# Kernel optimization log

Hardware: AMD Instinct MI355X
Metric: run time of the kernel (lower is better)

## Reference

```python
import jax, jax.numpy as jnp
import numpy as np

B, N, E = 128, 4096, 262144  # batch, num_vertices, num_edges


def setup_inputs() -> dict:
    key = jax.random.key(0)
    k1, k2, k3, k4, k5 = jax.random.split(key, 5)
    x = jax.random.normal(k1, (B, N), dtype=jnp.float32)
    error = jax.random.normal(k2, (B, N), dtype=jnp.float32)
    w = jax.random.normal(k3, (N, N), dtype=jnp.float32) * 0.02  # dense weight matrix, masked by adj in orig
    src = jax.random.randint(k4, (E,), 0, N)
    tgt = jax.random.randint(k5, (E,), 0, N)
    edge_index = jnp.stack([src, tgt]).astype(jnp.int32)  # [2, E]
    return {"x": x, "error": error, "w": w, "edge_index": edge_index}


def reference(x, error, w, edge_index):
    # Activation f = tanh, dfdx = 1 - tanh^2 (set_activation convention).
    src, tgt = edge_index[0], edge_index[1]
    w_e = w[src, tgt]  # per-edge weight gather, [E]

    # --- PredictionMessagePassing (flow='target_to_source', aggr='add') ---
    # message: f(x_j) * weight with x_j = x[tgt]; aggregated at src nodes.
    fx_t = jnp.tanh(x[:, tgt])                          # [B, E]
    mu = jnp.zeros_like(x).at[:, src].add(fx_t * w_e)   # scatter-add -> [B, N]

    # --- GradientMessagePassing (flow='source_to_target', aggr='add') ---
    # message: dfdx(x_i) * error_j * weight with x_i = x[tgt], error_j = error[src];
    # aggregated at tgt nodes; update: error - aggr_out.
    dfdx_t = 1.0 - fx_t * fx_t                          # [B, E]
    aggr = jnp.zeros_like(x).at[:, tgt].add(dfdx_t * error[:, src] * w_e)
    dEdx = error - aggr                                 # [B, N]

    return mu, dEdx
```

## Files before the change

kernel.cpp:

```cpp
#include <hip/hip_runtime.h>
#include <hip/hip_fp16.h>
#include <math.h>

#define B    128
#define NV   4096
#define NE   262144
#define CAP  192
#define KSC  128
#define EPB  2048
#define NS   8192
#define SCOLS 64


__device__ inline float2 h2f(unsigned u) {
    __half2 h;
    *reinterpret_cast<unsigned*>(&h) = u;
    return __half22float2(h);
}
__device__ inline __half2 u2h2(unsigned u) {
    __half2 h;
    *reinterpret_cast<unsigned*>(&h) = u;
    return h;
}

__global__ __launch_bounds__(256)
void k_hist(const int* __restrict__ ei, const float* __restrict__ w,
            unsigned* __restrict__ hist, ushort* __restrict__ wst) {
    __shared__ unsigned shm[NS];
    const int t = threadIdx.x, blk = blockIdx.x;
#pragma unroll
    for (int i = 0; i < NS / 256; ++i) shm[t + 256 * i] = 0u;
    __syncthreads();
    const int base = blk * EPB + t;
    int sn[8], tn[8];
#pragma unroll
    for (int i = 0; i < 8; ++i) {
        const int e = base + 256 * i;
        sn[i] = ei[e];
        tn[i] = ei[NE + e];
    }
    ushort wh[8];
#pragma unroll
    for (int i = 0; i < 8; ++i)
        wh[i] = __half_as_ushort(__float2half_rn(w[(size_t)sn[i] * NV + tn[i]]));
#pragma unroll
    for (int i = 0; i < 8; ++i) {
        atomicAdd(&shm[sn[i]], 1u);
        atomicAdd(&shm[4096 + tn[i]], 1u);
    }
#pragma unroll
    for (int i = 0; i < 8; ++i)
        wst[base + 256 * i] = wh[i];
    __syncthreads();
    unsigned* hrow = hist + (size_t)blk * NS;
#pragma unroll
    for (int i = 0; i < NS / 256; ++i) hrow[t + 256 * i] = shm[t + 256 * i];
}

__global__ __launch_bounds__(256)
void k_ts(const float* __restrict__ x, const float* __restrict__ err,
          ushort* __restrict__ Th, ushort* __restrict__ Eh,
          const unsigned* __restrict__ hist, unsigned* __restrict__ off,
          unsigned* __restrict__ count) {
    __shared__ unsigned shm[NS];
    const int t = threadIdx.x, blk = blockIdx.x;

    if (blk < 512) {
        float* tile0 = (float*)shm;
        float* tile1 = tile0 + 1056;
        const int n0 = (blk & 127) * 32;
        const int b0 = (blk >> 7) * 32;
        const int a = t & 31, c0 = t >> 5;
#pragma unroll
        for (int r = 0; r < 4; ++r) {
            int c = c0 + 8 * r;
            int gi = (b0 + c) * NV + (n0 + a);
            tile0[c * 33 + a] = tanhf(x[gi]);
            tile1[c * 33 + a] = err[gi];
        }
        __syncthreads();
#pragma unroll
        for (int r = 0; r < 4; ++r) {
            int c = c0 + 8 * r;
            int go = (n0 + c) * B + (b0 + a);
            Th[go] = __half_as_ushort(__float2half_rn(tile0[a * 33 + c]));
            Eh[go] = __half_as_ushort(__float2half_rn(tile1[a * 33 + c]));
        }
    } else {
        unsigned* p = shm;
        const int n0 = (blk - 512) * SCOLS;
#pragma unroll
        for (int i = 0; i < (KSC * SCOLS) / 256; ++i) {
            int l = t + 256 * i;
            p[l] = hist[(size_t)(l >> 6) * NS + n0 + (l & 63)];
        }
        __syncthreads();
        const int col = t >> 2, seg = t & 3;
        unsigned s = 0;
#pragma unroll
        for (int j = 0; j < KSC / 4; ++j) s += p[(seg * (KSC / 4) + j) * SCOLS + col];
        unsigned inc = s;
        unsigned v1 = __shfl_up(inc, 1, 4); if (seg >= 1) inc += v1;
        unsigned v2 = __shfl_up(inc, 2, 4); if (seg >= 2) inc += v2;
        unsigned run = inc - s;
        if (seg == 3) count[n0 + col] = inc;
#pragma unroll
        for (int j = 0; j < KSC / 4; ++j) {
            int idx = (seg * (KSC / 4) + j) * SCOLS + col;
            unsigned old = p[idx];
            p[idx] = run;
            run += old;
        }
        __syncthreads();
#pragma unroll
        for (int i = 0; i < (KSC * SCOLS) / 256; ++i) {
            int l = t + 256 * i;
            off[(size_t)(l >> 6) * NS + n0 + (l & 63)] = p[l];
        }
    }
}

__global__ __launch_bounds__(256)
void k_place(const int* __restrict__ ei, const ushort* __restrict__ wst,
             const unsigned* __restrict__ off,
             unsigned* __restrict__ es, unsigned* __restrict__ et) {
    __shared__ unsigned slot[NS];
    const int t = threadIdx.x, blk = blockIdx.x;
    const unsigned* orow = off + (size_t)blk * NS;
#pragma unroll
    for (int i = 0; i < NS / 256; ++i) slot[t + 256 * i] = orow[t + 256 * i];
    const int base = blk * EPB + t;
    int sn[8], tn[8];
    unsigned wh[8];
#pragma unroll
    for (int i = 0; i < 8; ++i) {
        const int e = base + 256 * i;
        sn[i] = ei[e];
        tn[i] = ei[NE + e];
        wh[i] = (unsigned)wst[e];
    }
    __syncthreads();
    unsigned pp[8], qq[8];
#pragma unroll
    for (int i = 0; i < 8; ++i) {
        pp[i] = atomicAdd(&slot[sn[i]], 1u);
        qq[i] = atomicAdd(&slot[4096 + tn[i]], 1u);
    }
#pragma unroll
    for (int i = 0; i < 8; ++i) {
        if (pp[i] < CAP) es[sn[i] * CAP + pp[i]] = ((unsigned)tn[i] << 16) | wh[i];
        if (qq[i] < CAP) et[tn[i] * CAP + qq[i]] = ((unsigned)sn[i] << 16) | wh[i];
    }
}

__global__ __launch_bounds__(64)
void k_proc(const unsigned* __restrict__ count,
            const unsigned* __restrict__ es, const unsigned* __restrict__ et,
            const unsigned* __restrict__ Th2, const unsigned* __restrict__ Eh2,
            float* __restrict__ out) {
    const int raw    = blockIdx.x;
    const bool is_mu = raw < NV;
    const int b2     = is_mu ? raw : raw - NV;
    const int node   = (b2 & 7) * (NV / 8) + (b2 >> 3);
    int n_e = (int)count[is_mu ? node : NV + node];
    if (n_e > CAP) n_e = CAP;
    const unsigned* ed  = (is_mu ? es : et) + node * CAP;
    const int4*     ed4 = (const int4*)ed;
    const unsigned* srcH = is_mu ? Th2 : Eh2;
    const int lane = threadIdx.x;

    __half2 a0 = u2h2(0u), a1 = u2h2(0u), a2 = u2h2(0u), a3 = u2h2(0u);
    __half2 a4 = u2h2(0u), a5 = u2h2(0u), a6 = u2h2(0u), a7 = u2h2(0u);
    int k = 0;
    for (; k + 16 <= n_e; k += 16) {
        int4 mA = ed4[(k >> 2) + 0];
        int4 mB = ed4[(k >> 2) + 1];
        int4 mC = ed4[(k >> 2) + 2];
        int4 mD = ed4[(k >> 2) + 3];
        const unsigned r0 = (unsigned)mA.x, r1 = (unsigned)mA.y;
        const unsigned r2 = (unsigned)mA.z, r3 = (unsigned)mA.w;
        const unsigned r4 = (unsigned)mB.x, r5 = (unsigned)mB.y;
        const unsigned r6 = (unsigned)mB.z, r7 = (unsigned)mB.w;
        const unsigned r8 = (unsigned)mC.x, r9 = (unsigned)mC.y;
        const unsigned rA = (unsigned)mC.z, rB = (unsigned)mC.w;
        const unsigned rC = (unsigned)mD.x, rD = (unsigned)mD.y;
        const unsigned rE = (unsigned)mD.z, rF = (unsigned)mD.w;
        unsigned g0 = srcH[(r0 >> 16) * (B / 2) + lane];
        unsigned g1 = srcH[(r1 >> 16) * (B / 2) + lane];
        unsigned g2 = srcH[(r2 >> 16) * (B / 2) + lane];
        unsigned g3 = srcH[(r3 >> 16) * (B / 2) + lane];
        unsigned g4 = srcH[(r4 >> 16) * (B / 2) + lane];
        unsigned g5 = srcH[(r5 >> 16) * (B / 2) + lane];
        unsigned g6 = srcH[(r6 >> 16) * (B / 2) + lane];
        unsigned g7 = srcH[(r7 >> 16) * (B / 2) + lane];
        unsigned g8 = srcH[(r8 >> 16) * (B / 2) + lane];
        unsigned g9 = srcH[(r9 >> 16) * (B / 2) + lane];
        unsigned gA = srcH[(rA >> 16) * (B / 2) + lane];
        unsigned gB = srcH[(rB >> 16) * (B / 2) + lane];
        unsigned gC = srcH[(rC >> 16) * (B / 2) + lane];
        unsigned gD = srcH[(rD >> 16) * (B / 2) + lane];
        unsigned gE = srcH[(rE >> 16) * (B / 2) + lane];
        unsigned gF = srcH[(rF >> 16) * (B / 2) + lane];
        a0 = __hfma2(u2h2(g0), u2h2(__builtin_amdgcn_perm(r0, r0, 0x01000100u)), a0);
        a1 = __hfma2(u2h2(g1), u2h2(__builtin_amdgcn_perm(r1, r1, 0x01000100u)), a1);
        a2 = __hfma2(u2h2(g2), u2h2(__builtin_amdgcn_perm(r2, r2, 0x01000100u)), a2);
        a3 = __hfma2(u2h2(g3), u2h2(__builtin_amdgcn_perm(r3, r3, 0x01000100u)), a3);
        a4 = __hfma2(u2h2(g4), u2h2(__builtin_amdgcn_perm(r4, r4, 0x01000100u)), a4);
        a5 = __hfma2(u2h2(g5), u2h2(__builtin_amdgcn_perm(r5, r5, 0x01000100u)), a5);
        a6 = __hfma2(u2h2(g6), u2h2(__builtin_amdgcn_perm(r6, r6, 0x01000100u)), a6);
        a7 = __hfma2(u2h2(g7), u2h2(__builtin_amdgcn_perm(r7, r7, 0x01000100u)), a7);
        a0 = __hfma2(u2h2(g8), u2h2(__builtin_amdgcn_perm(r8, r8, 0x01000100u)), a0);
        a1 = __hfma2(u2h2(g9), u2h2(__builtin_amdgcn_perm(r9, r9, 0x01000100u)), a1);
        a2 = __hfma2(u2h2(gA), u2h2(__builtin_amdgcn_perm(rA, rA, 0x01000100u)), a2);
        a3 = __hfma2(u2h2(gB), u2h2(__builtin_amdgcn_perm(rB, rB, 0x01000100u)), a3);
        a4 = __hfma2(u2h2(gC), u2h2(__builtin_amdgcn_perm(rC, rC, 0x01000100u)), a4);
        a5 = __hfma2(u2h2(gD), u2h2(__builtin_amdgcn_perm(rD, rD, 0x01000100u)), a5);
        a6 = __hfma2(u2h2(gE), u2h2(__builtin_amdgcn_perm(rE, rE, 0x01000100u)), a6);
        a7 = __hfma2(u2h2(gF), u2h2(__builtin_amdgcn_perm(rF, rF, 0x01000100u)), a7);
    }
    for (; k + 8 <= n_e; k += 8) {
        int4 mA = ed4[(k >> 2) + 0];
        int4 mB = ed4[(k >> 2) + 1];
        const unsigned r0 = (unsigned)mA.x, r1 = (unsigned)mA.y;
        const unsigned r2 = (unsigned)mA.z, r3 = (unsigned)mA.w;
        const unsigned r4 = (unsigned)mB.x, r5 = (unsigned)mB.y;
        const unsigned r6 = (unsigned)mB.z, r7 = (unsigned)mB.w;
        unsigned g0 = srcH[(r0 >> 16) * (B / 2) + lane];
        unsigned g1 = srcH[(r1 >> 16) * (B / 2) + lane];
        unsigned g2 = srcH[(r2 >> 16) * (B / 2) + lane];
        unsigned g3 = srcH[(r3 >> 16) * (B / 2) + lane];
        unsigned g4 = srcH[(r4 >> 16) * (B / 2) + lane];
        unsigned g5 = srcH[(r5 >> 16) * (B / 2) + lane];
        unsigned g6 = srcH[(r6 >> 16) * (B / 2) + lane];
        unsigned g7 = srcH[(r7 >> 16) * (B / 2) + lane];
        a0 = __hfma2(u2h2(g0), u2h2(__builtin_amdgcn_perm(r0, r0, 0x01000100u)), a0);
        a1 = __hfma2(u2h2(g1), u2h2(__builtin_amdgcn_perm(r1, r1, 0x01000100u)), a1);
        a2 = __hfma2(u2h2(g2), u2h2(__builtin_amdgcn_perm(r2, r2, 0x01000100u)), a2);
        a3 = __hfma2(u2h2(g3), u2h2(__builtin_amdgcn_perm(r3, r3, 0x01000100u)), a3);
        a4 = __hfma2(u2h2(g4), u2h2(__builtin_amdgcn_perm(r4, r4, 0x01000100u)), a4);
        a5 = __hfma2(u2h2(g5), u2h2(__builtin_amdgcn_perm(r5, r5, 0x01000100u)), a5);
        a6 = __hfma2(u2h2(g6), u2h2(__builtin_amdgcn_perm(r6, r6, 0x01000100u)), a6);
        a7 = __hfma2(u2h2(g7), u2h2(__builtin_amdgcn_perm(r7, r7, 0x01000100u)), a7);
    }
    for (; k < n_e; ++k) {
        unsigned r = ed[k];
        unsigned g = srcH[(r >> 16) * (B / 2) + lane];
        a0 = __hfma2(u2h2(g), u2h2(__builtin_amdgcn_perm(r, r, 0x01000100u)), a0);
    }
    float2 f0 = __half22float2(a0), f1 = __half22float2(a1);
    float2 f2 = __half22float2(a2), f3 = __half22float2(a3);
    float2 f4 = __half22float2(a4), f5 = __half22float2(a5);
    float2 f6 = __half22float2(a6), f7 = __half22float2(a7);
    f0.x += f1.x; f0.y += f1.y;  f2.x += f3.x; f2.y += f3.y;
    f4.x += f5.x; f4.y += f5.y;  f6.x += f7.x; f6.y += f7.y;
    f0.x += f2.x; f0.y += f2.y;  f4.x += f6.x; f4.y += f6.y;
    float2 acc = make_float2(f0.x + f4.x, f0.y + f4.y);

    const int b0 = 2 * lane;
    if (is_mu) {
        out[(size_t)b0 * NV + node]       = acc.x;
        out[(size_t)(b0 + 1) * NV + node] = acc.y;
    } else {
        const int oi = node * (B / 2) + lane;
        float2 th = h2f(Th2[oi]);
        float2 er = h2f(Eh2[oi]);
        float* o2 = out + (size_t)B * NV;
        o2[(size_t)b0 * NV + node]       = er.x - (1.f - th.x * th.x) * acc.x;
        o2[(size_t)(b0 + 1) * NV + node] = er.y - (1.f - th.y * th.y) * acc.y;
    }
}

extern "C" void kernel_launch(void* const* d_in, const int* in_sizes, int n_in,
                              void* d_out, int out_size, void* d_ws, size_t ws_size,
                              hipStream_t stream) {
    const float* x   = (const float*)d_in[0];
    const float* err = (const float*)d_in[1];
    const float* w   = (const float*)d_in[2];
    const int*   ei  = (const int*)d_in[3];
    float* out = (float*)d_out;

    const int NB = NV * B;
    ushort*   Th    = (ushort*)d_ws;
    ushort*   Eh    = Th + NB;
    ushort*   wst   = Eh + NB;
    unsigned* hist  = (unsigned*)(wst + NE);
    unsigned* off   = hist + (size_t)KSC * NS;
    unsigned* count = off + (size_t)KSC * NS;
    unsigned* es    = count + NS;
    unsigned* et    = es + (size_t)NV * CAP;

    k_hist<<<KSC, 256, 0, stream>>>(ei, w, hist, wst);
    k_ts<<<512 + KSC, 256, 0, stream>>>(x, err, Th, Eh, hist, off, count);
    k_place<<<KSC, 256, 0, stream>>>(ei, wst, off, es, et);
    k_proc<<<2 * NV, 64, 0, stream>>>(count, es, et,
                                      (const unsigned*)Th, (const unsigned*)Eh, out);
}
```

Baseline: 132.3 us.

## Fuse histogram, scan and placement kernels using in-kernel grid barriers

Merges the histogram, prefix-scan and edge-placement kernels into one launch that also does the x/error transpose. The 128 edge blocks synchronise through two atomic-counter barriers in global memory. Each edge block keeps its edge indices and half-precision weights in registers across the phases, so the intermediate weight buffer and two kernel launches go away. The barrier assumes the counters start at the workspace poison value and are never reset, and it assumes all 128 edge blocks are resident at the same time, which risks a hang or wrong ordering if either assumption fails.

After: 148.1 us. +11.9%, slower.

```diff
diff --git a/kernel.cpp b/kernel.cpp
--- a/kernel.cpp
+++ b/kernel.cpp
@@ -10,6 +10,7 @@
 #define EPB  2048
 #define NS   8192
 #define SCOLS 64
+#define POISON 0xAAAAAAAAu
 
 
 __device__ inline float2 h2f(unsigned u) {
@@ -23,45 +24,25 @@
     return h;
 }
 
+__device__ inline void barrier128(unsigned* ctr, int t) {
+    __syncthreads();
+    if (t == 0) {
+        __hip_atomic_fetch_add(ctr, 1u, __ATOMIC_ACQ_REL,
+                               __HIP_MEMORY_SCOPE_AGENT);
+        while (__hip_atomic_load(ctr, __ATOMIC_ACQUIRE,
+                                 __HIP_MEMORY_SCOPE_AGENT) - POISON < 128u)
+            __builtin_amdgcn_s_sleep(8);
+    }
+    __syncthreads();
+}
+
 __global__ __launch_bounds__(256)
-void k_hist(const int* __restrict__ ei, const float* __restrict__ w,
-            unsigned* __restrict__ hist, ushort* __restrict__ wst) {
-    __shared__ unsigned shm[NS];
-    const int t = threadIdx.x, blk = blockIdx.x;
-#pragma unroll
-    for (int i = 0; i < NS / 256; ++i) shm[t + 256 * i] = 0u;
-    __syncthreads();
-    const int base = blk * EPB + t;
-    int sn[8], tn[8];
-#pragma unroll
-    for (int i = 0; i < 8; ++i) {
-        const int e = base + 256 * i;
-        sn[i] = ei[e];
-        tn[i] = ei[NE + e];
-    }
-    ushort wh[8];
-#pragma unroll
-    for (int i = 0; i < 8; ++i)
-        wh[i] = __half_as_ushort(__float2half_rn(w[(size_t)sn[i] * NV + tn[i]]));
-#pragma unroll
-    for (int i = 0; i < 8; ++i) {
-        atomicAdd(&shm[sn[i]], 1u);
-        atomicAdd(&shm[4096 + tn[i]], 1u);
-    }
-#pragma unroll
-    for (int i = 0; i < 8; ++i)
-        wst[base + 256 * i] = wh[i];
-    __syncthreads();
-    unsigned* hrow = hist + (size_t)blk * NS;
-#pragma unroll
-    for (int i = 0; i < NS / 256; ++i) hrow[t + 256 * i] = shm[t + 256 * i];
-}
-
-__global__ __launch_bounds__(256)
-void k_ts(const float* __restrict__ x, const float* __restrict__ err,
-          ushort* __restrict__ Th, ushort* __restrict__ Eh,
-          const unsigned* __restrict__ hist, unsigned* __restrict__ off,
-          unsigned* __restrict__ count) {
+void k_build(const float* __restrict__ x, const float* __restrict__ err,
+             const float* __restrict__ w, const int* __restrict__ ei,
+             ushort* __restrict__ Th, ushort* __restrict__ Eh,
+             unsigned* __restrict__ hist, unsigned* __restrict__ off,
+             unsigned* __restrict__ count, unsigned* __restrict__ ctr,
+             unsigned* __restrict__ es, unsigned* __restrict__ et) {
     __shared__ unsigned shm[NS];
     const int t = threadIdx.x, blk = blockIdx.x;
 
@@ -86,9 +67,41 @@
             Th[go] = __half_as_ushort(__float2half_rn(tile0[a * 33 + c]));
             Eh[go] = __half_as_ushort(__float2half_rn(tile1[a * 33 + c]));
         }
-    } else {
+        return;
+    }
+
+    const int k2 = blk - 512;
+#pragma unroll
+    for (int i = 0; i < NS / 256; ++i) shm[t + 256 * i] = 0u;
+    __syncthreads();
+    const int base = k2 * EPB + t;
+    int sn[8], tn[8];
+#pragma unroll
+    for (int i = 0; i < 8; ++i) {
+        const int e = base + 256 * i;
+        sn[i] = ei[e];
+        tn[i] = ei[NE + e];
+    }
+    unsigned wh[8];
+#pragma unroll
+    for (int i = 0; i < 8; ++i)
+        wh[i] = (unsigned)__half_as_ushort(
+            __float2half_rn(w[(size_t)sn[i] * NV + tn[i]]));
+#pragma unroll
+    for (int i = 0; i < 8; ++i) {
+        atomicAdd(&shm[sn[i]], 1u);
+        atomicAdd(&shm[4096 + tn[i]], 1u);
+    }
+    __syncthreads();
+    unsigned* hrow = hist + (size_t)k2 * NS;
+#pragma unroll
+    for (int i = 0; i < NS / 256; ++i) hrow[t + 256 * i] = shm[t + 256 * i];
+
+    barrier128(&ctr[0], t);
+
+    {
         unsigned* p = shm;
-        const int n0 = (blk - 512) * SCOLS;
+        const int n0 = k2 * SCOLS;
 #pragma unroll
         for (int i = 0; i < (KSC * SCOLS) / 256; ++i) {
             int l = t + 256 * i;
@@ -118,33 +131,18 @@
             off[(size_t)(l >> 6) * NS + n0 + (l & 63)] = p[l];
         }
     }
-}
-
-__global__ __launch_bounds__(256)
-void k_place(const int* __restrict__ ei, const ushort* __restrict__ wst,
-             const unsigned* __restrict__ off,
-             unsigned* __restrict__ es, unsigned* __restrict__ et) {
-    __shared__ unsigned slot[NS];
-    const int t = threadIdx.x, blk = blockIdx.x;
-    const unsigned* orow = off + (size_t)blk * NS;
-#pragma unroll
-    for (int i = 0; i < NS / 256; ++i) slot[t + 256 * i] = orow[t + 256 * i];
-    const int base = blk * EPB + t;
-    int sn[8], tn[8];
-    unsigned wh[8];
-#pragma unroll
-    for (int i = 0; i < 8; ++i) {
-        const int e = base + 256 * i;
-        sn[i] = ei[e];
-        tn[i] = ei[NE + e];
-        wh[i] = (unsigned)wst[e];
-    }
+
+    barrier128(&ctr[16], t);
+
+    const unsigned* orow = off + (size_t)k2 * NS;
+#pragma unroll
+    for (int i = 0; i < NS / 256; ++i) shm[t + 256 * i] = orow[t + 256 * i];
     __syncthreads();
     unsigned pp[8], qq[8];
 #pragma unroll
     for (int i = 0; i < 8; ++i) {
-        pp[i] = atomicAdd(&slot[sn[i]], 1u);
-        qq[i] = atomicAdd(&slot[4096 + tn[i]], 1u);
+        pp[i] = atomicAdd(&shm[sn[i]], 1u);
+        qq[i] = atomicAdd(&shm[4096 + tn[i]], 1u);
     }
 #pragma unroll
     for (int i = 0; i < 8; ++i) {
@@ -282,16 +280,15 @@
     const int NB = NV * B;
     ushort*   Th    = (ushort*)d_ws;
     ushort*   Eh    = Th + NB;
-    ushort*   wst   = Eh + NB;
-    unsigned* hist  = (unsigned*)(wst + NE);
+    unsigned* hist  = (unsigned*)(Eh + NB);
     unsigned* off   = hist + (size_t)KSC * NS;
     unsigned* count = off + (size_t)KSC * NS;
-    unsigned* es    = count + NS;
+    unsigned* ctr   = count + NS;
+    unsigned* es    = ctr + 32;
     unsigned* et    = es + (size_t)NV * CAP;
 
-    k_hist<<<KSC, 256, 0, stream>>>(ei, w, hist, wst);
-    k_ts<<<512 + KSC, 256, 0, stream>>>(x, err, Th, Eh, hist, off, count);
-    k_place<<<KSC, 256, 0, stream>>>(ei, wst, off, es, et);
+    k_build<<<512 + KSC, 256, 0, stream>>>(x, err, w, ei, Th, Eh,
+                                           hist, off, count, ctr, es, et);
     k_proc<<<2 * NV, 64, 0, stream>>>(count, es, et,
                                       (const unsigned*)Th, (const unsigned*)Eh, out);
 }
```
